# Kernel tuning notes

Measured on AMD Instinct MI355X. Metric: run time of the kernel, lower is better.

## Reference

```python
import jax, jax.numpy as jnp
import numpy as np
from jax import lax

NMS_THRESH = 0.7
PRE_NMS_TOPK = 1000
POST_NMS_TOPK = 256
MIN_SIZE = 0.0


def setup_inputs() -> dict:
    key = jax.random.key(0)
    ks = jax.random.split(key, 4)
    N, C, Hf, Wf, P = 2, 128, 256, 256, 9
    x = jax.random.normal(ks[0], (N, C, Hf, Wf), jnp.float32)
    # small weight scales keep exp(offsets*stride) in a sane range (offsets head is zero-init in torch)
    W_conv = jax.random.normal(ks[1], (C, C, 3, 3), jnp.float32) * 0.05
    b_conv = jnp.zeros((C,), jnp.float32)
    W_off = jax.random.normal(ks[2], (2 * P, C), jnp.float32) * 0.01
    b_off = jnp.zeros((2 * P,), jnp.float32)
    W_log = jax.random.normal(ks[3], (1, C), jnp.float32) * 0.05
    b_log = jnp.zeros((1,), jnp.float32)
    return {"x": x, "W_conv": W_conv, "b_conv": b_conv, "W_off": W_off,
            "b_off": b_off, "W_log": W_log, "b_log": b_log,
            "image_h": 2048, "image_w": 2048}


def _forward_dense(x, W_conv, b_conv, W_off, b_off, W_log, b_log, image_h, image_w):
    N, C, Hf, Wf = x.shape
    t = lax.conv_general_dilated(x, W_conv, (1, 1), ((1, 1), (1, 1)),
                                 dimension_numbers=("NCHW", "OIHW", "NCHW"))
    t = jax.nn.relu(t + b_conv[None, :, None, None])
    logits = jnp.einsum("nchw,oc->nohw", t, W_log) + b_log[None, :, None, None]  # (N,1,Hf,Wf)
    off = jnp.einsum("nchw,oc->nohw", t, W_off) + b_off[None, :, None, None]      # (N,18,Hf,Wf)
    scale = image_w / Wf  # rescale() asserts scale_x == scale_y
    off = jnp.exp(off * scale) - 1.0
    # offsets2coordinates -- faithful to the torch code, including the H/W linspace
    # swap (ys spans image W over Hf points, xs spans image H over Wf points);
    # benign for square images.
    ys_lin = jnp.linspace(0.0, image_w - 1.0, Hf)
    xs_lin = jnp.linspace(0.0, image_h - 1.0, Wf)
    ys = jnp.broadcast_to(ys_lin[:, None], (Hf, Wf))
    xs = jnp.broadcast_to(xs_lin[None, :], (Hf, Wf))
    coords = off.reshape(N, 9, 2, Hf, Wf) + jnp.stack([xs, ys], 0)[None, None]
    cx = jnp.clip(coords[:, :, 0], 0.0, image_w - 1.0)  # clamp(0, W-1)
    cy = jnp.clip(coords[:, :, 1], 0.0, image_h - 1.0)  # clamp(0, H-1)
    # predict_proposals: min/max over the 9 points -> [N, Hf*Wf, 4]
    boxes = jnp.stack([cx.min(1), cy.min(1), cx.max(1), cy.max(1)], -1).reshape(N, Hf * Wf, 4)
    scores = logits.reshape(N, Hf * Wf)
    return scores, boxes


def _iou_matrix(b):
    x1, y1, x2, y2 = b[:, 0], b[:, 1], b[:, 2], b[:, 3]
    area = (x2 - x1) * (y2 - y1)
    iw = jnp.clip(jnp.minimum(x2[:, None], x2[None, :]) - jnp.maximum(x1[:, None], x1[None, :]), 0.0)
    ih = jnp.clip(jnp.minimum(y2[:, None], y2[None, :]) - jnp.maximum(y1[:, None], y1[None, :]), 0.0)
    inter = iw * ih
    return inter / (area[:, None] + area[None, :] - inter + 1e-9)


def _nms_one_image(scores, boxes):
    # pre-NMS topk (scores already returned sorted descending by top_k)
    sc, idx = lax.top_k(scores, PRE_NMS_TOPK)
    b = boxes[idx]
    w = b[:, 2] - b[:, 0]
    h = b[:, 3] - b[:, 1]
    valid = (w >= MIN_SIZE) & (h >= MIN_SIZE)
    sc = jnp.where(valid, sc, -jnp.inf)
    iou = _iou_matrix(b)
    ar = jnp.arange(PRE_NMS_TOPK)

    def body(i, sup):
        alive = (~sup[i]) & valid[i]
        return sup | ((iou[i] > NMS_THRESH) & (ar > i) & alive)

    sup = lax.fori_loop(0, PRE_NMS_TOPK, body, jnp.zeros((PRE_NMS_TOPK,), bool))
    keep_sc = jnp.where(sup, -jnp.inf, sc)
    final_sc, fidx = lax.top_k(keep_sc, POST_NMS_TOPK)
    return b[fidx], final_sc


def reference(x, W_conv, b_conv, W_off, b_off, W_log, b_log, image_h, image_w):
    scores, boxes = _forward_dense(x, W_conv, b_conv, W_off, b_off, W_log, b_log, image_h, image_w)
    out = jnp.concatenate([scores[..., None], boxes], axis=-1)  # (N, Hf*Wf, 5)
    kept_boxes, kept_scores = jax.vmap(_nms_one_image)(scores, boxes)
    return out, kept_boxes, kept_scores
```

## Files before the change

kernel.cpp:

```cpp
#include <hip/hip_runtime.h>
#include <stdint.h>

typedef unsigned int u32;
typedef unsigned long long u64;
typedef __attribute__((ext_vector_type(4))) short short4v;
typedef __attribute__((ext_vector_type(8))) short short8;
typedef __attribute__((ext_vector_type(16))) float f32x16;

#define DEVI __device__ __forceinline__

constexpr int PRE_K = 1000;
constexpr int CAP = 8192;

constexpr size_t WF_OFF    = 0;
constexpr size_t HIST_OFF  = 884736;
constexpr size_t CNT_OFF   = 917504;
constexpr size_t CUT_OFF   = 917568;
constexpr size_t CAND_OFF  = 917632;
constexpr size_t TB_OFF    = 1048704;
constexpr size_t SCS_OFF   = 1080704;
constexpr size_t MASK_OFF  = 1088768;
constexpr size_t SCARR_OFF = 1350912;
constexpr size_t WS_NEED   = 1875200;

constexpr size_t KB_OFF = 655360;
constexpr size_t KS_OFF = 657408;

DEVI u32 fkey(float f) {
  u32 u = __float_as_uint(f);
  return (u & 0x80000000u) ? ~u : (u | 0x80000000u);
}

DEVI u64 shfl64(u64 v, int src) {
  int lo = __shfl((int)(u32)v, src, 64);
  int hi = __shfl((int)(u32)(v >> 32), src, 64);
  return ((u64)(u32)hi << 32) | (u64)(u32)lo;
}

DEVI u32 rne16(u32 u) { return (u + 0x7FFFu + ((u >> 16) & 1u)) >> 16; }

__global__ void wsplitk(const float* __restrict__ wc, float* __restrict__ wf,
                        u32* __restrict__ hist, u32* __restrict__ cnt) {
  int j = blockIdx.x * 256 + threadIdx.x;
  if (j < 8192) hist[j] = 0;
  if (j < 2) cnt[j] = 0;
  if (j >= 18432) return;
  int co = j / 144;
  int koct = j % 144;
  short8 h8, m8, l8;
#pragma unroll
  for (int jj = 0; jj < 8; ++jj) {
    int kk = koct * 8 + jj;
    int tap = kk >> 7, ci = kk & 127;
    float v = wc[(co * 128 + ci) * 9 + tap];
    u32 u0 = __float_as_uint(v);
    u32 hb = rne16(u0);
    float r1 = v - __uint_as_float(hb << 16);
    u32 mb = rne16(__float_as_uint(r1));
    float r2 = r1 - __uint_as_float(mb << 16);
    u32 lb = rne16(__float_as_uint(r2));
    h8[jj] = (short)hb; m8[jj] = (short)mb; l8[jj] = (short)lb;
  }
  int slot = ((koct & 1) << 5) + (co & 31);
  int kg = koct >> 1;
  int cblk = co >> 5;
  char* base = (char*)wf;
  *(short8*)(base + ((size_t)((0 * 4 + cblk) * 72 + kg) * 64 + slot) * 16) = h8;
  *(short8*)(base + ((size_t)((1 * 4 + cblk) * 72 + kg) * 64 + slot) * 16) = m8;
  *(short8*)(base + ((size_t)((2 * 4 + cblk) * 72 + kg) * 64 + slot) * 16) = l8;
}

__global__ __launch_bounds__(256, 2) void convk(
    const float* __restrict__ x, const float* __restrict__ wf,
    const float* __restrict__ bconv,
    const float* __restrict__ woff, const float* __restrict__ boff,
    const float* __restrict__ wlog, const float* __restrict__ blog,
    const int* __restrict__ ihp, const int* __restrict__ iwp,
    float* __restrict__ out, u32* __restrict__ hist, float* __restrict__ scarr)
{
  __shared__ union {
    unsigned short pl[3 * 3600];
    float tq[32][132];
  } sm;

  const int tid = threadIdx.x;
  const int l = tid & 63, wv = tid >> 6;
  const int mhalf = wv >> 1, nhalf = wv & 1;
  const int lm = l & 31, lg = l >> 5;
  const int bx = blockIdx.x, by = blockIdx.y, n = blockIdx.z;

  f32x16 acc[2][2];
#pragma unroll
  for (int mi = 0; mi < 2; ++mi)
#pragma unroll
    for (int ni = 0; ni < 2; ++ni)
#pragma unroll
      for (int q = 0; q < 16; ++q) acc[mi][ni][q] = 0.f;

  const char* wfb = (const char*)wf;

#pragma unroll 1
  for (int cc = 0; cc < 8; ++cc) {
    __syncthreads();
    const float* xbase = x + ((size_t)n * 128 + cc * 16) * 65536;
    for (int e = tid; e < 2880; e += 256) {
      int ci = e / 180, rem = e % 180;
      int hh = rem / 18, ww = rem % 18;
      int gh = by * 8 + hh - 1, gw = bx * 16 + ww - 1;
      float v = 0.f;
      if ((unsigned)gh < 256u && (unsigned)gw < 256u)
        v = xbase[(size_t)ci * 65536 + gh * 256 + gw];
      u32 u0 = __float_as_uint(v);
      u32 hb = rne16(u0);
      float r1 = v - __uint_as_float(hb << 16);
      u32 mb = rne16(__float_as_uint(r1));
      float r2 = r1 - __uint_as_float(mb << 16);
      u32 lb = rne16(__float_as_uint(r2));
      int idx = (hh * 18 + ww) * 20 + ci;
      sm.pl[idx] = (unsigned short)hb;
      sm.pl[idx + 3600] = (unsigned short)mb;
      sm.pl[idx + 7200] = (unsigned short)lb;
    }
    __syncthreads();

#pragma unroll 1
    for (int tap = 0; tap < 9; ++tap) {
      int dy = tap / 3 - 1, dx = tap % 3 - 1;
      short8 Af[3][2];
#pragma unroll
      for (int mi = 0; mi < 2; ++mi) {
        int hh = mhalf * 4 + mi * 2 + (lm >> 4) + dy + 1;
        int ww = (lm & 15) + dx + 1;
        int base = (hh * 18 + ww) * 20 + lg * 8;
#pragma unroll
        for (int s = 0; s < 3; ++s) {
          short4v a0 = *(const short4v*)&sm.pl[s * 3600 + base];
          short4v a1 = *(const short4v*)&sm.pl[s * 3600 + base + 4];
          short8 v8 = {a0[0], a0[1], a0[2], a0[3], a1[0], a1[1], a1[2], a1[3]};
          Af[s][mi] = v8;
        }
      }
#pragma unroll
      for (int sb = 0; sb < 3; ++sb) {
        short8 Bf[2];
#pragma unroll
        for (int ni = 0; ni < 2; ++ni) {
          int fid = (sb * 4 + nhalf * 2 + ni) * 72 + tap * 8 + cc;
          Bf[ni] = *(const short8*)(wfb + ((size_t)fid * 64 + l) * 16);
        }
#pragma unroll
        for (int sa = 0; sa < 3 - sb; ++sa)
#pragma unroll
          for (int mi = 0; mi < 2; ++mi)
#pragma unroll
            for (int ni = 0; ni < 2; ++ni)
              acc[mi][ni] = __builtin_amdgcn_mfma_f32_32x32x16_bf16(
                  Af[sa][mi], Bf[ni], acc[mi][ni], 0, 0, 0);
      }
    }
  }

  __syncthreads();
  const int ihv = ihp[0], iwv = iwp[0];
  float bcv[2];
  bcv[0] = bconv[nhalf * 64 + lm];
  bcv[1] = bconv[nhalf * 64 + 32 + lm];
  const int cq = l >> 4;
  const int pxl = (nhalf << 4) + (l & 15);
  const float scale = (float)iwv / 256.0f;

#pragma unroll 1
  for (int mh = 0; mh < 2; ++mh) {
#pragma unroll 1
    for (int r = 0; r < 2; ++r) {
      if (mh || r) __syncthreads();
      if (mhalf == mh) {
#pragma unroll
        for (int ni = 0; ni < 2; ++ni)
#pragma unroll
          for (int rg = 0; rg < 16; ++rg) {
            int row = (rg & 3) + ((rg >> 2) << 3) + ((l >> 5) << 2);
            sm.tq[row][(nhalf << 6) + (ni << 5) + lm] =
                fmaxf((r ? acc[1][ni][rg] : acc[0][ni][rg]) + bcv[ni], 0.f);
          }
      }
      __syncthreads();
      if (mhalf == mh) {
        float tv[32];
#pragma unroll
        for (int i = 0; i < 8; ++i) {
          float4 t4 = *(const float4*)&sm.tq[pxl][(cq << 5) + (i << 2)];
          tv[i * 4 + 0] = t4.x; tv[i * 4 + 1] = t4.y;
          tv[i * 4 + 2] = t4.z; tv[i * 4 + 3] = t4.w;
        }
        float s19[19];
#pragma unroll
        for (int o = 0; o < 19; ++o) {
          const float* wh = (o < 18) ? (woff + o * 128) : wlog;
          const float4* w4 = (const float4*)(wh + (cq << 5));
          float a0 = 0.f;
#pragma unroll
          for (int i = 0; i < 8; ++i) {
            float4 wv4 = w4[i];
            a0 = fmaf(tv[i * 4 + 0], wv4.x, a0);
            a0 = fmaf(tv[i * 4 + 1], wv4.y, a0);
            a0 = fmaf(tv[i * 4 + 2], wv4.z, a0);
            a0 = fmaf(tv[i * 4 + 3], wv4.w, a0);
          }
          s19[o] = a0;
        }
#pragma unroll
        for (int o = 0; o < 19; ++o) {
          s19[o] += __shfl_xor(s19[o], 16, 64);
          s19[o] += __shfl_xor(s19[o], 32, 64);
        }
        if (cq == 0) {
          int bpx = (mh << 6) + (r << 5) + pxl;
          int ph = bpx >> 4, pw = bpx & 15;
          int gh = by * 8 + ph, gw = bx * 16 + pw;
          float sc = s19[18] + blog[0];
          float xv = (float)((double)gw * ((double)(ihv - 1) / 255.0));
          float yv = (float)((double)gh * ((double)(iwv - 1) / 255.0));
          float mnx = __builtin_inff(), mny = __builtin_inff();
          float mxx = -__builtin_inff(), mxy = -__builtin_inff();
#pragma unroll
          for (int p = 0; p < 9; ++p) {
            float ox = expf((s19[2 * p] + boff[2 * p]) * scale) - 1.f + xv;
            float oy = expf((s19[2 * p + 1] + boff[2 * p + 1]) * scale) - 1.f + yv;
            float cx2 = fminf(fmaxf(ox, 0.f), (float)(iwv - 1));
            float cy2 = fminf(fmaxf(oy, 0.f), (float)(ihv - 1));
            mnx = fminf(mnx, cx2); mxx = fmaxf(mxx, cx2);
            mny = fminf(mny, cy2); mxy = fmaxf(mxy, cy2);
          }
          size_t pix = (size_t)n * 65536 + (size_t)gh * 256 + gw;
          float* rec = out + pix * 5;
          rec[0] = sc; rec[1] = mnx; rec[2] = mny; rec[3] = mxx; rec[4] = mxy;
          if (scarr) scarr[pix] = sc;
          atomicAdd(&hist[n * 4096 + (fkey(sc) >> 20)], 1u);
        }
      }
    }
  }
}

__global__ __launch_bounds__(256) void cutoffk(const u32* __restrict__ hist, u32* __restrict__ cut) {
  int n = blockIdx.x;
  const u32* h = hist + n * 4096;
  __shared__ u32 pre[256];
  int t = threadIdx.x;
  u32 s0 = 0;
  for (int k = 0; k < 16; ++k) s0 += h[4095 - (t * 16 + k)];
  pre[t] = s0;
  __syncthreads();
  for (int off = 1; off < 256; off <<= 1) {
    u32 add = (t >= off) ? pre[t - off] : 0u;
    __syncthreads();
    pre[t] += add;
    __syncthreads();
  }
  u32 incl = pre[t];
  u32 excl = incl - s0;
  if (incl >= (u32)PRE_K && excl < (u32)PRE_K) {
    u32 cum = excl;
    for (int k = 0; k < 16; ++k) {
      int b = 4095 - (t * 16 + k);
      cum += h[b];
      if (cum >= (u32)PRE_K) { cut[n] = ((u32)b) << 20; break; }
    }
  }
}

__global__ void collectk(const float* __restrict__ out, const float* __restrict__ scarr,
                         const u32* __restrict__ cut,
                         u32* __restrict__ cnt, u64* __restrict__ cand) {
  int e = blockIdx.x * 256 + threadIdx.x;
  int n = e >> 16;
  u32 pix = e & 65535;
  float sc = scarr ? scarr[e] : out[((size_t)n * 65536 + pix) * 5];
  u32 key = fkey(sc);
  if (key >= cut[n]) {
    u32 pos = atomicAdd(&cnt[n], 1u);
    if (pos < (u32)CAP)
      cand[(size_t)n * CAP + pos] = ((u64)key << 32) | (u64)(0xFFFFFFFFu - pix);
  }
}

__global__ __launch_bounds__(1024) void ranksel(const u64* __restrict__ cand, const u32* __restrict__ cnt,
                                                const float* __restrict__ out,
                                                float* __restrict__ tb, float* __restrict__ scs) {
  int n = blockIdx.x;
  int t = threadIdx.x;
  __shared__ u64 d[CAP];
  u32 m = cnt[n]; if (m > (u32)CAP) m = CAP;
  for (int i = t; i < (int)m; i += 1024) d[i] = cand[(size_t)n * CAP + i];
  __syncthreads();
  for (int i = t; i < (int)m; i += 1024) {
    u64 ki = d[i];
    u32 r = 0;
    for (u32 j = 0; j < m; ++j) r += (d[j] > ki) ? 1u : 0u;
    if (r < (u32)PRE_K) {
      u32 pix = 0xFFFFFFFFu - (u32)(ki & 0xFFFFFFFFull);
      const float* rec = out + ((size_t)n * 65536 + pix) * 5;
      float sc = rec[0];
      float b0 = rec[1], b1 = rec[2], b2 = rec[3], b3 = rec[4];
      bool valid = ((b2 - b0) >= 0.f) && ((b3 - b1) >= 0.f);
      scs[n * PRE_K + r] = valid ? sc : -__builtin_inff();
      float* tbp = tb + ((size_t)n * PRE_K + r) * 4;
      tbp[0] = b0; tbp[1] = b1; tbp[2] = b2; tbp[3] = b3;
    }
  }
}

__global__ __launch_bounds__(1024) void maskk(const float* __restrict__ tb, u64* __restrict__ maskw) {
  int c = blockIdx.x;
  int n = blockIdx.y;
  int t = threadIdx.x;
  __shared__ float bx[PRE_K][4];
  for (int e = t; e < PRE_K * 4; e += 1024) ((float*)bx)[e] = tb[(size_t)n * PRE_K * 4 + e];
  __syncthreads();
  u64 accm = 0;
  if (t < PRE_K) {
    float x1 = bx[t][0], y1 = bx[t][1], x2 = bx[t][2], y2 = bx[t][3];
    float ai = (x2 - x1) * (y2 - y1);
    int j0 = max(t + 1, c * 64), j1 = min(PRE_K, c * 64 + 64);
    for (int j = j0; j < j1; ++j) {
      float u1 = bx[j][0], v1 = bx[j][1], u2 = bx[j][2], v2 = bx[j][3];
      float aj = (u2 - u1) * (v2 - v1);
      float iw = fminf(x2, u2) - fmaxf(x1, u1); iw = fmaxf(iw, 0.f);
      float ih = fminf(y2, v2) - fmaxf(y1, v1); ih = fmaxf(ih, 0.f);
      float inter = iw * ih;
      float iou = inter / (ai + aj - inter + 1e-9f);
      if (iou > 0.7f) accm |= (1ull << (j & 63));
    }
  }
  maskw[((size_t)n * 1024 + t) * 16 + c] = accm;
}

__global__ __launch_bounds__(64) void finalk(const u64* __restrict__ maskw,
                                             const float* __restrict__ scs,
                                             const float* __restrict__ tb,
                                             float* __restrict__ out) {
  int n = blockIdx.x;
  int lane = threadIdx.x;
  __shared__ float lsc[1024];
  __shared__ unsigned short ordA[1024];
  __shared__ unsigned short ordB[1024];
  for (int e = lane; e < 1024; e += 64)
    lsc[e] = (e < PRE_K) ? scs[n * PRE_K + e] : -__builtin_inff();
  __syncthreads();

  u64 sup = 0;
#pragma unroll
  for (int c = 0; c < 16; ++c) {
    u64 b = __ballot(!(lsc[c * 64 + lane] > -__builtin_inff()));
    if (lane == c) sup = b;
  }

  const u64* gm = maskw + (size_t)n * 1024 * 16;
  u64 pre[16];
#pragma unroll
  for (int d = 0; d < 16; ++d)
    pre[d] = (lane < 16) ? gm[d * 16 + lane] : 0ull;

  for (int i0 = 0; i0 < 1024; i0 += 16) {
#pragma unroll
    for (int d = 0; d < 16; ++d) {
      int i = i0 + d;
      u64 mi = pre[d];
      int nx = i + 16;
      pre[d] = (nx < 1024 && lane < 16) ? gm[(size_t)nx * 16 + lane] : 0ull;
      int w = i >> 6;
      u64 sw = shfl64(sup, w);
      bool supbit = (sw >> (i & 63)) & 1ull;
      if (!supbit) sup |= mi;
    }
  }

  u64 ltm = (1ull << lane) - 1ull;
  u32 baseA = 0, baseB = 0;
  for (int c = 0; c < 16; ++c) {
    int i = c * 64 + lane;
    u64 sw = shfl64(sup, c);
    bool bit = (sw >> lane) & 1ull;
    bool vi = i < PRE_K;
    bool sf = vi && !bit && (lsc[vi ? i : 0] > -__builtin_inff());
    u64 mA = __ballot(sf);
    u64 mB = __ballot(vi && !sf);
    if (sf) ordA[baseA + __popcll(mA & ltm)] = (unsigned short)i;
    else if (vi) ordB[baseB + __popcll(mB & ltm)] = (unsigned short)i;
    baseA += (u32)__popcll(mA);
    baseB += (u32)__popcll(mB);
  }
  __syncthreads();

  for (int r = 0; r < 4; ++r) {
    int k = r * 64 + lane;
    int fi; float v;
    if (k < (int)baseA) { fi = ordA[k]; v = lsc[fi]; }
    else { fi = ordB[k - baseA]; v = -__builtin_inff(); }
    const float* bp = tb + ((size_t)n * PRE_K + fi) * 4;
    float* kb = out + KB_OFF + ((size_t)n * 256 + k) * 4;
    kb[0] = bp[0]; kb[1] = bp[1]; kb[2] = bp[2]; kb[3] = bp[3];
    out[KS_OFF + (size_t)n * 256 + k] = v;
  }
}

extern "C" void kernel_launch(void* const* d_in, const int* in_sizes, int n_in,
                              void* d_out, int out_size, void* d_ws, size_t ws_size,
                              hipStream_t stream) {
  const float* x     = (const float*)d_in[0];
  const float* wc    = (const float*)d_in[1];
  const float* bconv = (const float*)d_in[2];
  const float* woff  = (const float*)d_in[3];
  const float* boff  = (const float*)d_in[4];
  const float* wlog  = (const float*)d_in[5];
  const float* blog  = (const float*)d_in[6];
  const int* ihp     = (const int*)d_in[7];
  const int* iwp     = (const int*)d_in[8];
  float* out = (float*)d_out;
  char* ws = (char*)d_ws;

  float* wf    = (float*)(ws + WF_OFF);
  u32* hist    = (u32*)(ws + HIST_OFF);
  u32* cnt     = (u32*)(ws + CNT_OFF);
  u32* cut     = (u32*)(ws + CUT_OFF);
  u64* cand    = (u64*)(ws + CAND_OFF);
  float* tb    = (float*)(ws + TB_OFF);
  float* scs   = (float*)(ws + SCS_OFF);
  u64* maskw   = (u64*)(ws + MASK_OFF);
  float* scarr = (ws_size >= WS_NEED) ? (float*)(ws + SCARR_OFF) : nullptr;

  hipLaunchKernelGGL(wsplitk, dim3(72), dim3(256), 0, stream, wc, wf, hist, cnt);
  hipLaunchKernelGGL(convk, dim3(16, 32, 2), dim3(256), 0, stream,
                     x, wf, bconv, woff, boff, wlog, blog, ihp, iwp, out, hist, scarr);
  hipLaunchKernelGGL(cutoffk, dim3(2), dim3(256), 0, stream, hist, cut);
  hipLaunchKernelGGL(collectk, dim3(512), dim3(256), 0, stream, out, scarr, cut, cnt, cand);
  hipLaunchKernelGGL(ranksel, dim3(2), dim3(1024), 0, stream, cand, cnt, out, tb, scs);
  hipLaunchKernelGGL(maskk, dim3(16, 2), dim3(1024), 0, stream, tb, maskw);
  hipLaunchKernelGGL(finalk, dim3(2), dim3(64), 0, stream, maskw, scs, tb, out);
}
```

Baseline: 654.8 us.

## Prefetch next input channel chunk into registers during MFMA compute

The conv kernel now issues global loads for the next 16-channel input chunk into registers before running the 9-tap MFMA loop on the current chunk. Once compute finishes, it splits the staged values into bf16 hi/mid/lo parts and writes them to shared memory. This hides global load latency behind matrix work. The cost is 24 extra live registers per thread, which may lower occupancy or cause spills in a kernel already holding large accumulators.

```diff
diff --git a/kernel.cpp b/kernel.cpp
--- a/kernel.cpp
+++ b/kernel.cpp
@@ -99,29 +99,54 @@
 
   const char* wfb = (const char*)wf;
 
+  float stv[12];
+  int stix[12];
+
+#define STAGE_ISSUE(CC)                                                        \
+  {                                                                            \
+    const float* xbase = x + ((size_t)n * 128 + (CC) * 16) * 65536;            \
+    _Pragma("unroll")                                                          \
+    for (int k = 0; k < 12; ++k) {                                             \
+      int e = tid + (k << 8);                                                  \
+      float v = 0.f; int ix = -1;                                              \
+      if (e < 2880) {                                                          \
+        int ci = e / 180, rem = e % 180;                                       \
+        int hh = rem / 18, ww = rem % 18;                                      \
+        int gh = by * 8 + hh - 1, gw = bx * 16 + ww - 1;                       \
+        if ((unsigned)gh < 256u && (unsigned)gw < 256u)                        \
+          v = xbase[(size_t)ci * 65536 + gh * 256 + gw];                       \
+        ix = (hh * 18 + ww) * 20 + ci;                                         \
+      }                                                                        \
+      stv[k] = v; stix[k] = ix;                                                \
+    }                                                                          \
+  }
+
+#define STAGE_WRITE()                                                          \
+  {                                                                            \
+    _Pragma("unroll")                                                          \
+    for (int k = 0; k < 12; ++k) {                                             \
+      if (stix[k] >= 0) {                                                      \
+        float v = stv[k];                                                      \
+        u32 u0 = __float_as_uint(v);                                           \
+        u32 hb = rne16(u0);                                                    \
+        float r1 = v - __uint_as_float(hb << 16);                              \
+        u32 mb = rne16(__float_as_uint(r1));                                   \
+        float r2 = r1 - __uint_as_float(mb << 16);                             \
+        u32 lb = rne16(__float_as_uint(r2));                                   \
+        sm.pl[stix[k]] = (unsigned short)hb;                                   \
+        sm.pl[stix[k] + 3600] = (unsigned short)mb;                            \
+        sm.pl[stix[k] + 7200] = (unsigned short)lb;                            \
+      }                                                                        \
+    }                                                                          \
+  }
+
+  STAGE_ISSUE(0);
+  STAGE_WRITE();
+  __syncthreads();
+
 #pragma unroll 1
   for (int cc = 0; cc < 8; ++cc) {
-    __syncthreads();
-    const float* xbase = x + ((size_t)n * 128 + cc * 16) * 65536;
-    for (int e = tid; e < 2880; e += 256) {
-      int ci = e / 180, rem = e % 180;
-      int hh = rem / 18, ww = rem % 18;
-      int gh = by * 8 + hh - 1, gw = bx * 16 + ww - 1;
-      float v = 0.f;
-      if ((unsigned)gh < 256u && (unsigned)gw < 256u)
-        v = xbase[(size_t)ci * 65536 + gh * 256 + gw];
-      u32 u0 = __float_as_uint(v);
-      u32 hb = rne16(u0);
-      float r1 = v - __uint_as_float(hb << 16);
-      u32 mb = rne16(__float_as_uint(r1));
-      float r2 = r1 - __uint_as_float(mb << 16);
-      u32 lb = rne16(__float_as_uint(r2));
-      int idx = (hh * 18 + ww) * 20 + ci;
-      sm.pl[idx] = (unsigned short)hb;
-      sm.pl[idx + 3600] = (unsigned short)mb;
-      sm.pl[idx + 7200] = (unsigned short)lb;
-    }
-    __syncthreads();
+    if (cc < 7) STAGE_ISSUE(cc + 1);
 
 #pragma unroll 1
     for (int tap = 0; tap < 9; ++tap) {
@@ -157,6 +182,12 @@
               acc[mi][ni] = __builtin_amdgcn_mfma_f32_32x32x16_bf16(
                   Af[sa][mi], Bf[ni], acc[mi][ni], 0, 0, 0);
       }
+    }
+
+    __syncthreads();
+    if (cc < 7) {
+      STAGE_WRITE();
+      __syncthreads();
     }
   }
 
@@ -241,6 +272,8 @@
       }
     }
   }
+#undef STAGE_ISSUE
+#undef STAGE_WRITE
 }
 
 __global__ __launch_bounds__(256) void cutoffk(const u32* __restrict__ hist, u32* __restrict__ cut) {
```

Measured after the change: 609.9 us. -6.9%, faster.
